# Performance work log

Hardware: AMD Instinct MI355X
Metric: run time of the kernel (lower is better)

Reference implementation:

```python
import jax, jax.numpy as jnp
import numpy as np

BATCH = 64
INPUT_LENGTH = 128
N_TERMINALS = 64
N_NONTERMINALS = 128


def setup_inputs() -> dict:
    key = jax.random.key(0)
    k1, k2, k3 = jax.random.split(key, 3)
    input_tensor = jax.random.uniform(k1, (BATCH, INPUT_LENGTH, N_TERMINALS), dtype=jnp.float32)
    terminal_productions = jax.random.normal(k2, (N_NONTERMINALS, N_TERMINALS), dtype=jnp.float32)
    nonterminal_productions = jax.random.normal(k3, (N_NONTERMINALS, N_NONTERMINALS, N_TERMINALS), dtype=jnp.float32)
    return {
        "input_tensor": input_tensor,
        "terminal_productions": terminal_productions,
        "nonterminal_productions": nonterminal_productions,
    }


def reference(input_tensor, terminal_productions, nonterminal_productions):
    # input_tensor: [B, L, T]
    tp = jax.nn.sigmoid(terminal_productions)            # [N, T]
    ntp = jax.nn.sigmoid(nonterminal_productions)        # [N, N, T]

    # step 0: terminal production choices
    tpc = jnp.einsum('nt,bt->bn', tp, input_tensor[:, 0])  # [B, N]
    out0 = tpc[:, 0]                                        # [B]

    def step(carry, x_i):
        prev_choices, prev_out = carry                     # [B, N], [B]
        # per-batch nonterminal production choice matrix: [B, N, N]
        npc = jnp.clip(jnp.einsum('nmt,bt->bnm', ntp, x_i), 0.0, 1.0)
        cur = jnp.clip(jnp.einsum('bnm,bm->bn', npc, prev_choices), 0.0, 1.0)
        mask = x_i[:, N_TERMINALS - 1]                     # [B]
        out = prev_out * mask + cur[:, 0] * (1.0 - mask)
        return (cur, out), None

    xs = jnp.swapaxes(input_tensor[:, 1:], 0, 1)           # [L-1, B, T]
    (final_choices, final_out), _ = jax.lax.scan(step, (tpc, out0), xs)
    return final_out[:, None]                              # [B, 1]
```

## Files before the change

### kernel.cpp

```cpp
#include <hip/hip_runtime.h>
#include <hip/hip_bf16.h>

typedef unsigned int u32;
typedef unsigned char u8;
typedef _Float16 f16;
typedef f16 f16x2 __attribute__((ext_vector_type(2)));
typedef short s16x8 __attribute__((ext_vector_type(8)));
typedef float f32x4 __attribute__((ext_vector_type(4)));

#define BB 64
#define LL 128
#define TT 64
#define NN 128
#define NM (NN*NN)

__device__ __forceinline__ float sigf(float v) {
    return 1.0f / (1.0f + __expf(-v));
}

__device__ __forceinline__ float clip01(float v) {
    return fminf(fmaxf(v, 0.f), 1.f);
}

__device__ __forceinline__ u32 f2bf(float f) {
    u32 u = __builtin_bit_cast(u32, f);
    return (u + 0x7fffu + ((u >> 16) & 1u)) >> 16;
}

__device__ __forceinline__ float fdot2f(f16x2 wa, f16x2 xa, float ca) {
#if defined(__HIP_DEVICE_COMPILE__) && __has_builtin(__builtin_amdgcn_fdot2)
    return __builtin_amdgcn_fdot2(wa, xa, ca, false);
#else
    return ca + (float)wa[0] * (float)xa[0] + (float)wa[1] * (float)xa[1];
#endif
}

__device__ __forceinline__ u32 ud4(u32 a, u32 b, u32 c) {
#if defined(__HIP_DEVICE_COMPILE__) && __has_builtin(__builtin_amdgcn_udot4)
    return __builtin_amdgcn_udot4(a, b, c, false);
#else
    return c + (a & 255u) * (b & 255u) + ((a >> 8) & 255u) * ((b >> 8) & 255u)
             + ((a >> 16) & 255u) * ((b >> 16) & 255u) + (a >> 24) * (b >> 24);
#endif
}

__global__ __launch_bounds__(256) void pack_w(const float* __restrict__ ntp,
                                              ushort* __restrict__ wpk) {
    const int g = blockIdx.x * 256 + threadIdx.x;
    const int l = g & 63, h = (g >> 6) & 1, i = g >> 7;
    const int row = i * 16 + (l & 15);
    const int t0 = h * 32 + ((l >> 4) << 3);
    const float* src = ntp + row * 64 + t0;
    float4 f0 = *reinterpret_cast<const float4*>(src);
    float4 f1 = *reinterpret_cast<const float4*>(src + 4);
    float v[8] = {f0.x, f0.y, f0.z, f0.w, f1.x, f1.y, f1.z, f1.w};
    u32 o[4];
    #pragma unroll
    for (int q = 0; q < 4; ++q)
        o[q] = f2bf(sigf(v[2 * q])) | (f2bf(sigf(v[2 * q + 1])) << 16);
    uint4 ov; ov.x = o[0]; ov.y = o[1]; ov.z = o[2]; ov.w = o[3];
    *reinterpret_cast<uint4*>(wpk + (size_t)g * 8) = ov;
}

__global__ __launch_bounds__(256) void pack_x(const float* __restrict__ x_all,
                                              ushort* __restrict__ xpk) {
    const int g = blockIdx.x * 256 + threadIdx.x;
    const int l = g & 63, h = (g >> 6) & 1, j = (g >> 7) & 7, b = g >> 10;
    const int s = j * 16 + (l & 15);
    const int t0 = h * 32 + ((l >> 4) << 3);
    const float* src = x_all + ((size_t)b * LL + s) * TT + t0;
    float4 f0 = *reinterpret_cast<const float4*>(src);
    float4 f1 = *reinterpret_cast<const float4*>(src + 4);
    float v[8] = {f0.x, f0.y, f0.z, f0.w, f1.x, f1.y, f1.z, f1.w};
    u32 o[4];
    #pragma unroll
    for (int q = 0; q < 4; ++q)
        o[q] = f2bf(v[2 * q]) | (f2bf(v[2 * q + 1]) << 16);
    uint4 ov; ov.x = o[0]; ov.y = o[1]; ov.z = o[2]; ov.w = o[3];
    *reinterpret_cast<uint4*>(xpk + (size_t)g * 8) = ov;
}

__global__ __launch_bounds__(256) void gemm_mfma(const ushort* __restrict__ wpk,
                                                 const ushort* __restrict__ xpk,
                                                 u8* __restrict__ npc) {
    __shared__ __align__(16) u8 stg[4][16384];
    const int b = blockIdx.x >> 4;
    const int nb = blockIdx.x & 15;
    const int wv = threadIdx.x >> 6, l = threadIdx.x & 63;

    uint4 xf[8][2];
    #pragma unroll
    for (int j = 0; j < 8; ++j)
        #pragma unroll
        for (int h = 0; h < 2; ++h)
            xf[j][h] = *reinterpret_cast<const uint4*>(
                xpk + (size_t)(((b * 8 + j) * 2 + h) * 64 + l) * 8);

    const int c = l & 15, r0 = (l >> 4) * 4;
    u8* stw = stg[wv];
    const int khi  = (nb >> 3) * 8;
    const int nlow = (nb & 7) * 8;

    for (int mg2 = 0; mg2 < 2; ++mg2) {
        const int mg = wv * 2 + mg2;
        #pragma unroll
        for (int n_l = 0; n_l < 8; ++n_l) {
            const int i = (nb * 8 + n_l) * 8 + mg;
            uint4 a0 = *reinterpret_cast<const uint4*>(wpk + (size_t)((i * 2 + 0) * 64 + l) * 8);
            uint4 a1 = *reinterpret_cast<const uint4*>(wpk + (size_t)((i * 2 + 1) * 64 + l) * 8);
            const f32x4 z = {0.f, 0.f, 0.f, 0.f};
            f32x4 acc[8];
            #pragma unroll
            for (int j = 0; j < 8; ++j)
                acc[j] = __builtin_amdgcn_mfma_f32_16x16x32_bf16(
                    __builtin_bit_cast(s16x8, a0), __builtin_bit_cast(s16x8, xf[j][0]), z, 0, 0, 0);
            #pragma unroll
            for (int j = 0; j < 8; ++j)
                acc[j] = __builtin_amdgcn_mfma_f32_16x16x32_bf16(
                    __builtin_bit_cast(s16x8, a1), __builtin_bit_cast(s16x8, xf[j][1]), acc[j], 0, 0, 0);

            const int sk = (((n_l + c) & 7) << 4) + r0;
            #pragma unroll
            for (int j = 0; j < 8; ++j) {
                u32 w = 0;
                #pragma unroll
                for (int r = 0; r < 4; ++r) {
                    float q = clip01(acc[j][r]) * 255.f + 0.5f;
                    w |= ((u32)q) << (8 * r);
                }
                *reinterpret_cast<u32*>(stw + j * 2048 + c * 128 + sk) = w;
            }
        }
        asm volatile("s_waitcnt lgkmcnt(0)" ::: "memory");
        __builtin_amdgcn_sched_barrier(0);

        const int nr = l & 7;
        #pragma unroll
        for (int j = 0; j < 8; ++j) {
            #pragma unroll
            for (int half = 0; half < 2; ++half) {
                const int cc = half * 8 + (l >> 3);
                uint4 v = *reinterpret_cast<const uint4*>(
                    stw + j * 2048 + cc * 128 + (((nr + cc) & 7) << 4));
                *reinterpret_cast<uint4*>(npc + ((size_t)b << 21) + ((size_t)j << 18)
                    + ((size_t)cc << 14) + ((size_t)(mg + khi) << 10)
                    + ((nlow + nr) << 4)) = v;
            }
        }
        asm volatile("s_waitcnt lgkmcnt(0)" ::: "memory");
        __builtin_amdgcn_sched_barrier(0);
    }
}

__global__ __launch_bounds__(256, 1) void recur8(const float* __restrict__ x_all,
                                                 const float* __restrict__ tp,
                                                 const u8* __restrict__ npc,
                                                 float* __restrict__ outp) {
    __shared__ __align__(16) u8 prev_lds[2][NN];
    __shared__ float masks_lds[LL];
    __shared__ float tpc_lds[NN];
    __shared__ float x0_lds[TT];

    const int b = blockIdx.x, tid = threadIdx.x;
    const int n = tid >> 1, h = tid & 1;
    const int koff = (n >> 6) * 8 + h * 4;
    const u8* npcl = npc + ((size_t)b << 21) + (u32)koff * 1024 + (u32)(n & 63) * 16;

    if (tid < 128) masks_lds[tid] = x_all[(size_t)b * 8192 + tid * 64 + 63];
    else if (tid < 192) x0_lds[tid - 128] = x_all[(size_t)b * 8192 + (tid - 128)];
    __syncthreads();

#define LOADSET(R, T) do { \
        int _t = (T) <= 127 ? (T) : 127; \
        const u8* _p = npcl + ((size_t)(_t >> 4) << 18) + ((size_t)(_t & 15) << 14); \
        R[0] = *reinterpret_cast<const uint4*>(_p); \
        R[1] = *reinterpret_cast<const uint4*>(_p + 1024); \
        R[2] = *reinterpret_cast<const uint4*>(_p + 2048); \
        R[3] = *reinterpret_cast<const uint4*>(_p + 3072); \
        asm volatile("" ::: "memory"); \
    } while (0)

    uint4 nA[4], nB[4], nC[4], nD[4];
    LOADSET(nA, 1); LOADSET(nB, 2); LOADSET(nC, 3); LOADSET(nD, 4);

    float out_r = 0.f;
    if (tid < 128) {
        float a = 0.f;
        #pragma unroll
        for (int t4 = 0; t4 < 16; ++t4) {
            float4 xv = *reinterpret_cast<const float4*>(x0_lds + t4 * 4);
            float4 w0 = *reinterpret_cast<const float4*>(tp + tid * 64 + t4 * 4);
            a += sigf(w0.x) * xv.x; a += sigf(w0.y) * xv.y;
            a += sigf(w0.z) * xv.z; a += sigf(w0.w) * xv.w;
        }
        tpc_lds[tid] = a;
        if (tid == 0) out_r = a;
    }
    asm volatile("s_waitcnt lgkmcnt(0)" ::: "memory");
    __builtin_amdgcn_s_barrier();
    __builtin_amdgcn_sched_barrier(0);

    {
        float sf = 0.f;
        #pragma unroll
        for (int j = 0; j < 4; ++j) {
            u32 cw[4] = {nA[j].x, nA[j].y, nA[j].z, nA[j].w};
            #pragma unroll
            for (int w = 0; w < 4; ++w) {
                float4 tv = *reinterpret_cast<const float4*>(
                    tpc_lds + h * 64 + j * 16 + w * 4);
                u32 aw = cw[w];
                sf += (float)(aw & 255u) * tv.x + (float)((aw >> 8) & 255u) * tv.y
                    + (float)((aw >> 16) & 255u) * tv.z + (float)(aw >> 24) * tv.w;
            }
        }
        float tot = sf + __shfl_xor(sf, 1);
        float c0 = clip01(tot * (1.f / 255.f));
        if (h == 0) prev_lds[0][n] = (u8)(c0 * 255.f + 0.5f);
        if (tid == 0) {
            float mk = masks_lds[1];
            out_r = out_r * mk + c0 * (1.f - mk);
        }
        asm volatile("s_waitcnt lgkmcnt(0)" ::: "memory");
        __builtin_amdgcn_s_barrier();
        __builtin_amdgcn_sched_barrier(0);
    }
    LOADSET(nA, 5);

    int p = 0;

#define STEP(R, S) do { \
        uint4 pv[4]; \
        _Pragma("unroll") \
        for (int _q = 0; _q < 4; ++_q) \
            pv[_q] = *reinterpret_cast<const uint4*>(&prev_lds[p][h * 64 + _q * 16]); \
        float mk = masks_lds[(S)]; \
        u32 s0 = 0, s1 = 0; \
        s0 = ud4(R[0].x, pv[0].x, s0); s0 = ud4(R[0].y, pv[0].y, s0); \
        s0 = ud4(R[0].z, pv[0].z, s0); s0 = ud4(R[0].w, pv[0].w, s0); \
        s1 = ud4(R[1].x, pv[1].x, s1); s1 = ud4(R[1].y, pv[1].y, s1); \
        s1 = ud4(R[1].z, pv[1].z, s1); s1 = ud4(R[1].w, pv[1].w, s1); \
        s0 = ud4(R[2].x, pv[2].x, s0); s0 = ud4(R[2].y, pv[2].y, s0); \
        s0 = ud4(R[2].z, pv[2].z, s0); s0 = ud4(R[2].w, pv[2].w, s0); \
        s1 = ud4(R[3].x, pv[3].x, s1); s1 = ud4(R[3].y, pv[3].y, s1); \
        s1 = ud4(R[3].z, pv[3].z, s1); s1 = ud4(R[3].w, pv[3].w, s1); \
        float sf = (float)(s0 + s1); \
        float tot = sf + __shfl_xor(sf, 1); \
        float c0 = fminf(tot * (1.f / 65025.f), 1.f); \
        if (h == 0) prev_lds[p ^ 1][n] = (u8)(c0 * 255.f + 0.5f); \
        if (tid == 0) out_r = out_r * mk + c0 * (1.f - mk); \
        asm volatile("s_waitcnt lgkmcnt(0)" ::: "memory"); \
        __builtin_amdgcn_s_barrier(); \
        __builtin_amdgcn_sched_barrier(0); \
        p ^= 1; \
    } while (0)

    for (int g = 0; g < 31; ++g) {
        const int s = 2 + 4 * g;
        STEP(nB, s);     LOADSET(nB, s + 4);
        STEP(nC, s + 1); LOADSET(nC, s + 5);
        STEP(nD, s + 2); LOADSET(nD, s + 6);
        STEP(nA, s + 3); LOADSET(nA, s + 7);
    }
    STEP(nB, 126);
    STEP(nC, 127);

#undef STEP
#undef LOADSET

    if (tid == 0) outp[b] = out_r;
}

__global__ __launch_bounds__(256) void sig_transpose(const float* __restrict__ ntp,
                                                     u32* __restrict__ out) {
    __shared__ float lds[64 * 65];
    const int nm0 = blockIdx.x * 64;
    const int tid = threadIdx.x;
    #pragma unroll
    for (int it = 0; it < 16; ++it) {
        int idx = it * 256 + tid;
        int r = idx >> 6, c = idx & 63;
        lds[r * 65 + c] = sigf(ntp[(nm0 + r) * 64 + c]);
    }
    __syncthreads();
    #pragma unroll
    for (int it = 0; it < 8; ++it) {
        int o = it * 256 + tid;
        int tpi = o >> 6, r = o & 63;
        f16x2 h;
        h[0] = (f16)lds[r * 65 + 2 * tpi];
        h[1] = (f16)lds[r * 65 + 2 * tpi + 1];
        out[tpi * NM + nm0 + r] = __builtin_bit_cast(u32, h);
    }
}

__global__ __launch_bounds__(1024) void grammar_fused(
    const float* __restrict__ x_all,
    const float* __restrict__ tp,
    const u32*  __restrict__ ntpT2,
    float* __restrict__ outp) {
    __shared__ float x_lds[LL * TT];
    __shared__ float prevbuf[2][NN];
    __shared__ u32 x2_lds[2][32];

    const int b = blockIdx.x;
    const int tid = threadIdx.x;
    const int lane16 = tid & 15;
    const int g = tid >> 4;
    const int mbase = lane16 * 8;

    const float* xb = x_all + b * (LL * TT);
    #pragma unroll
    for (int it = 0; it < 8; ++it) {
        int idx = it * 1024 + tid;
        x_lds[idx] = xb[idx];
    }
    __syncthreads();

    if (tid < NN) {
        float acc = 0.f;
        #pragma unroll 8
        for (int t = 0; t < TT; ++t)
            acc += sigf(tp[tid * TT + t]) * x_lds[t];
        prevbuf[0][tid] = acc;
    }
    __syncthreads();
    float out_r = 0.f;
    if (tid == 0) out_r = prevbuf[0][0];

    int p = 0;
    for (int i0 = 1; i0 < LL; i0 += 2) {
        const int ns = (LL - i0) >= 2 ? 2 : 1;
        if (tid < 64) {
            int s = tid >> 5, tpi = tid & 31;
            f16x2 h;
            if (s < ns) {
                h[0] = (f16)x_lds[(i0 + s) * TT + 2 * tpi];
                h[1] = (f16)x_lds[(i0 + s) * TT + 2 * tpi + 1];
            } else {
                h[0] = (f16)0.f; h[1] = (f16)0.f;
            }
            x2_lds[s][tpi] = __builtin_bit_cast(u32, h);
        }
        __syncthreads();

        float acc[2][2][8];
        #pragma unroll
        for (int k = 0; k < 2; ++k)
            #pragma unroll
            for (int s = 0; s < 2; ++s)
                #pragma unroll
                for (int j = 0; j < 8; ++j) acc[k][s][j] = 0.f;

        #pragma unroll 2
        for (int tpi = 0; tpi < 32; ++tpi) {
            f16x2 xv0 = __builtin_bit_cast(f16x2, x2_lds[0][tpi]);
            f16x2 xv1 = __builtin_bit_cast(f16x2, x2_lds[1][tpi]);
            const u32* base = ntpT2 + tpi * NM + 8 * tid;
            #pragma unroll
            for (int k = 0; k < 2; ++k) {
                uint4 w0 = *reinterpret_cast<const uint4*>(base + 8192 * k);
                uint4 w1 = *reinterpret_cast<const uint4*>(base + 8192 * k + 4);
                u32 wv[8] = {w0.x, w0.y, w0.z, w0.w, w1.x, w1.y, w1.z, w1.w};
                #pragma unroll
                for (int j = 0; j < 8; ++j) {
                    f16x2 w = __builtin_bit_cast(f16x2, wv[j]);
                    acc[k][0][j] = fdot2f(w, xv0, acc[k][0][j]);
                    acc[k][1][j] = fdot2f(w, xv1, acc[k][1][j]);
                }
            }
        }

        for (int s = 0; s < ns; ++s) {
            float4 pv0 = *reinterpret_cast<const float4*>(&prevbuf[p][mbase]);
            float4 pv1 = *reinterpret_cast<const float4*>(&prevbuf[p][mbase + 4]);
            float pvv[8] = {pv0.x, pv0.y, pv0.z, pv0.w, pv1.x, pv1.y, pv1.z, pv1.w};
            #pragma unroll
            for (int k = 0; k < 2; ++k) {
                float part = 0.f;
                #pragma unroll
                for (int j = 0; j < 8; ++j) {
                    float npcv = clip01(acc[k][s][j]);
                    part += npcv * pvv[j];
                }
                part += __shfl_xor(part, 1);
                part += __shfl_xor(part, 2);
                part += __shfl_xor(part, 4);
                part += __shfl_xor(part, 8);
                if (lane16 == 0) {
                    float c = clip01(part);
                    prevbuf[p ^ 1][g + 64 * k] = c;
                    if (tid == 0 && k == 0) {
                        float mask = x_lds[(i0 + s) * TT + 63];
                        out_r = out_r * mask + c * (1.f - mask);
                    }
                }
            }
            p ^= 1;
            __syncthreads();
        }
    }

    if (tid == 0) outp[b] = out_r;
}

extern "C" void kernel_launch(void* const* d_in, const int* in_sizes, int n_in,
                              void* d_out, int out_size, void* d_ws, size_t ws_size,
                              hipStream_t stream) {
    const float* input_tensor = (const float*)d_in[0];
    const float* term_prod    = (const float*)d_in[1];
    const float* nonterm_prod = (const float*)d_in[2];
    float* outp = (float*)d_out;

    const size_t MB = 1024 * 1024;
    const size_t NPC_BYTES = 128 * MB;
    const size_t WPK_BYTES = 2 * MB;
    const size_t XPK_BYTES = 1 * MB;

    if (ws_size >= NPC_BYTES + WPK_BYTES + XPK_BYTES + MB) {
        u8* npcbuf  = (u8*)d_ws;
        ushort* wpk = (ushort*)((char*)d_ws + NPC_BYTES);
        ushort* xpk = (ushort*)((char*)d_ws + NPC_BYTES + WPK_BYTES);
        pack_w<<<512, 256, 0, stream>>>(nonterm_prod, wpk);
        pack_x<<<256, 256, 0, stream>>>(input_tensor, xpk);
        gemm_mfma<<<1024, 256, 0, stream>>>(wpk, xpk, npcbuf);
        recur8<<<BB, 256, 0, stream>>>(input_tensor, term_prod, npcbuf, outp);
    } else {
        u32* ntpT2 = (u32*)d_ws;
        sig_transpose<<<256, 256, 0, stream>>>(nonterm_prod, ntpT2);
        grammar_fused<<<BB, 1024, 0, stream>>>(input_tensor, term_prod, ntpT2, outp);
    }
}
```

Baseline: 81.12 us.

## Quantize npc matrices to 4-bit nibbles and merge pack kernels

Stores the per-step choice matrices as 4-bit values (0..15) instead of 8-bit, halving the 128MB intermediate buffer written by the GEMM and streamed by the recurrence. The recurrence unpacks nibbles with masks/shifts into udot4 against a reordered packed prev vector. It also merges the two packing kernels into one launch. The coarser quantization adds precision error to the recurrent result.

```diff
diff --git a/kernel.cpp b/kernel.cpp
--- a/kernel.cpp
+++ b/kernel.cpp
@@ -44,46 +44,48 @@
 #endif
 }
 
-__global__ __launch_bounds__(256) void pack_w(const float* __restrict__ ntp,
-                                              ushort* __restrict__ wpk) {
-    const int g = blockIdx.x * 256 + threadIdx.x;
-    const int l = g & 63, h = (g >> 6) & 1, i = g >> 7;
-    const int row = i * 16 + (l & 15);
-    const int t0 = h * 32 + ((l >> 4) << 3);
-    const float* src = ntp + row * 64 + t0;
-    float4 f0 = *reinterpret_cast<const float4*>(src);
-    float4 f1 = *reinterpret_cast<const float4*>(src + 4);
-    float v[8] = {f0.x, f0.y, f0.z, f0.w, f1.x, f1.y, f1.z, f1.w};
-    u32 o[4];
-    #pragma unroll
-    for (int q = 0; q < 4; ++q)
-        o[q] = f2bf(sigf(v[2 * q])) | (f2bf(sigf(v[2 * q + 1])) << 16);
-    uint4 ov; ov.x = o[0]; ov.y = o[1]; ov.z = o[2]; ov.w = o[3];
-    *reinterpret_cast<uint4*>(wpk + (size_t)g * 8) = ov;
-}
-
-__global__ __launch_bounds__(256) void pack_x(const float* __restrict__ x_all,
-                                              ushort* __restrict__ xpk) {
-    const int g = blockIdx.x * 256 + threadIdx.x;
-    const int l = g & 63, h = (g >> 6) & 1, j = (g >> 7) & 7, b = g >> 10;
-    const int s = j * 16 + (l & 15);
-    const int t0 = h * 32 + ((l >> 4) << 3);
-    const float* src = x_all + ((size_t)b * LL + s) * TT + t0;
-    float4 f0 = *reinterpret_cast<const float4*>(src);
-    float4 f1 = *reinterpret_cast<const float4*>(src + 4);
-    float v[8] = {f0.x, f0.y, f0.z, f0.w, f1.x, f1.y, f1.z, f1.w};
-    u32 o[4];
-    #pragma unroll
-    for (int q = 0; q < 4; ++q)
-        o[q] = f2bf(v[2 * q]) | (f2bf(v[2 * q + 1]) << 16);
-    uint4 ov; ov.x = o[0]; ov.y = o[1]; ov.z = o[2]; ov.w = o[3];
-    *reinterpret_cast<uint4*>(xpk + (size_t)g * 8) = ov;
+__global__ __launch_bounds__(256) void pack_wx(const float* __restrict__ ntp,
+                                               const float* __restrict__ x_all,
+                                               ushort* __restrict__ wpk,
+                                               ushort* __restrict__ xpk) {
+    const int bid = blockIdx.x;
+    if (bid < 512) {
+        const int g = bid * 256 + threadIdx.x;
+        const int l = g & 63, h = (g >> 6) & 1, i = g >> 7;
+        const int row = i * 16 + (l & 15);
+        const int t0 = h * 32 + ((l >> 4) << 3);
+        const float* src = ntp + row * 64 + t0;
+        float4 f0 = *reinterpret_cast<const float4*>(src);
+        float4 f1 = *reinterpret_cast<const float4*>(src + 4);
+        float v[8] = {f0.x, f0.y, f0.z, f0.w, f1.x, f1.y, f1.z, f1.w};
+        u32 o[4];
+        #pragma unroll
+        for (int q = 0; q < 4; ++q)
+            o[q] = f2bf(sigf(v[2 * q])) | (f2bf(sigf(v[2 * q + 1])) << 16);
+        uint4 ov; ov.x = o[0]; ov.y = o[1]; ov.z = o[2]; ov.w = o[3];
+        *reinterpret_cast<uint4*>(wpk + (size_t)g * 8) = ov;
+    } else {
+        const int g = (bid - 512) * 256 + threadIdx.x;
+        const int l = g & 63, h = (g >> 6) & 1, j = (g >> 7) & 7, b = g >> 10;
+        const int s = j * 16 + (l & 15);
+        const int t0 = h * 32 + ((l >> 4) << 3);
+        const float* src = x_all + ((size_t)b * LL + s) * TT + t0;
+        float4 f0 = *reinterpret_cast<const float4*>(src);
+        float4 f1 = *reinterpret_cast<const float4*>(src + 4);
+        float v[8] = {f0.x, f0.y, f0.z, f0.w, f1.x, f1.y, f1.z, f1.w};
+        u32 o[4];
+        #pragma unroll
+        for (int q = 0; q < 4; ++q)
+            o[q] = f2bf(v[2 * q]) | (f2bf(v[2 * q + 1]) << 16);
+        uint4 ov; ov.x = o[0]; ov.y = o[1]; ov.z = o[2]; ov.w = o[3];
+        *reinterpret_cast<uint4*>(xpk + (size_t)g * 8) = ov;
+    }
 }
 
 __global__ __launch_bounds__(256) void gemm_mfma(const ushort* __restrict__ wpk,
                                                  const ushort* __restrict__ xpk,
                                                  u8* __restrict__ npc) {
-    __shared__ __align__(16) u8 stg[4][16384];
+    __shared__ __align__(16) u8 stg[4][8192];
     const int b = blockIdx.x >> 4;
     const int nb = blockIdx.x & 15;
     const int wv = threadIdx.x >> 6, l = threadIdx.x & 63;
@@ -119,32 +121,32 @@
                 acc[j] = __builtin_amdgcn_mfma_f32_16x16x32_bf16(
                     __builtin_bit_cast(s16x8, a1), __builtin_bit_cast(s16x8, xf[j][1]), acc[j], 0, 0, 0);
 
-            const int sk = (((n_l + c) & 7) << 4) + r0;
+            const int sk8 = ((n_l + c) & 7) << 3;
             #pragma unroll
             for (int j = 0; j < 8; ++j) {
-                u32 w = 0;
-                #pragma unroll
-                for (int r = 0; r < 4; ++r) {
-                    float q = clip01(acc[j][r]) * 255.f + 0.5f;
-                    w |= ((u32)q) << (8 * r);
-                }
-                *reinterpret_cast<u32*>(stw + j * 2048 + c * 128 + sk) = w;
+                u32 q0 = (u32)(clip01(acc[j][0]) * 15.f + 0.5f);
+                u32 q1 = (u32)(clip01(acc[j][1]) * 15.f + 0.5f);
+                u32 q2 = (u32)(clip01(acc[j][2]) * 15.f + 0.5f);
+                u32 q3 = (u32)(clip01(acc[j][3]) * 15.f + 0.5f);
+                u32 hw = (q0 | (q1 << 4)) | ((q2 | (q3 << 4)) << 8);
+                *reinterpret_cast<ushort*>(stw + j * 1024 + c * 64 + sk8 + (r0 >> 1)) = (ushort)hw;
             }
         }
         asm volatile("s_waitcnt lgkmcnt(0)" ::: "memory");
         __builtin_amdgcn_sched_barrier(0);
 
-        const int nr = l & 7;
         #pragma unroll
         for (int j = 0; j < 8; ++j) {
             #pragma unroll
-            for (int half = 0; half < 2; ++half) {
-                const int cc = half * 8 + (l >> 3);
-                uint4 v = *reinterpret_cast<const uint4*>(
-                    stw + j * 2048 + cc * 128 + (((nr + cc) & 7) << 4));
-                *reinterpret_cast<uint4*>(npc + ((size_t)b << 21) + ((size_t)j << 18)
-                    + ((size_t)cc << 14) + ((size_t)(mg + khi) << 10)
-                    + ((nlow + nr) << 4)) = v;
+            for (int r = 0; r < 2; ++r) {
+                const int slot = r * 64 + l;
+                const int cc = slot >> 3;
+                const int nr = slot & 7;
+                uint2 v = *reinterpret_cast<const uint2*>(
+                    stw + j * 1024 + cc * 64 + (((nr + cc) & 7) << 3));
+                *reinterpret_cast<uint2*>(npc + ((size_t)b << 20) + ((size_t)j << 17)
+                    + ((size_t)cc << 13) + ((size_t)(mg + khi) << 9)
+                    + ((nlow + nr) << 3)) = v;
             }
         }
         asm volatile("s_waitcnt lgkmcnt(0)" ::: "memory");
@@ -152,19 +154,19 @@
     }
 }
 
-__global__ __launch_bounds__(256, 1) void recur8(const float* __restrict__ x_all,
+__global__ __launch_bounds__(256, 1) void recur9(const float* __restrict__ x_all,
                                                  const float* __restrict__ tp,
                                                  const u8* __restrict__ npc,
                                                  float* __restrict__ outp) {
-    __shared__ __align__(16) u8 prev_lds[2][NN];
+    __shared__ u32 prev_pk[2][32];
     __shared__ float masks_lds[LL];
     __shared__ float tpc_lds[NN];
     __shared__ float x0_lds[TT];
 
     const int b = blockIdx.x, tid = threadIdx.x;
     const int n = tid >> 1, h = tid & 1;
-    const int koff = (n >> 6) * 8 + h * 4;
-    const u8* npcl = npc + ((size_t)b << 21) + (u32)koff * 1024 + (u32)(n & 63) * 16;
+    const u8* npcl = npc + ((size_t)b << 20)
+                   + ((size_t)((n >> 6) * 8 + h * 4) << 9) + (u32)(n & 63) * 8;
 
     if (tid < 128) masks_lds[tid] = x_all[(size_t)b * 8192 + tid * 64 + 63];
     else if (tid < 192) x0_lds[tid - 128] = x_all[(size_t)b * 8192 + (tid - 128)];
@@ -172,15 +174,15 @@
 
 #define LOADSET(R, T) do { \
         int _t = (T) <= 127 ? (T) : 127; \
-        const u8* _p = npcl + ((size_t)(_t >> 4) << 18) + ((size_t)(_t & 15) << 14); \
-        R[0] = *reinterpret_cast<const uint4*>(_p); \
-        R[1] = *reinterpret_cast<const uint4*>(_p + 1024); \
-        R[2] = *reinterpret_cast<const uint4*>(_p + 2048); \
-        R[3] = *reinterpret_cast<const uint4*>(_p + 3072); \
+        const u8* _p = npcl + ((size_t)(_t >> 4) << 17) + ((size_t)(_t & 15) << 13); \
+        R[0] = *reinterpret_cast<const uint2*>(_p); \
+        R[1] = *reinterpret_cast<const uint2*>(_p + 512); \
+        R[2] = *reinterpret_cast<const uint2*>(_p + 1024); \
+        R[3] = *reinterpret_cast<const uint2*>(_p + 1536); \
         asm volatile("" ::: "memory"); \
     } while (0)
 
-    uint4 nA[4], nB[4], nC[4], nD[4];
+    uint2 nA[4], nB[4], nC[4], nD[4];
     LOADSET(nA, 1); LOADSET(nB, 2); LOADSET(nC, 3); LOADSET(nD, 4);
 
     float out_r = 0.f;
@@ -200,23 +202,31 @@
     __builtin_amdgcn_s_barrier();
     __builtin_amdgcn_sched_barrier(0);
 
+    const int wr_idx  = ((n >> 4) << 1) + ((n >> 3) & 1) + ((n & 1) << 4);
+    const int wr_byte = (n & 7) >> 1;
+
     {
         float sf = 0.f;
         #pragma unroll
-        for (int j = 0; j < 4; ++j) {
-            u32 cw[4] = {nA[j].x, nA[j].y, nA[j].z, nA[j].w};
-            #pragma unroll
-            for (int w = 0; w < 4; ++w) {
-                float4 tv = *reinterpret_cast<const float4*>(
-                    tpc_lds + h * 64 + j * 16 + w * 4);
-                u32 aw = cw[w];
-                sf += (float)(aw & 255u) * tv.x + (float)((aw >> 8) & 255u) * tv.y
-                    + (float)((aw >> 16) & 255u) * tv.z + (float)(aw >> 24) * tv.w;
+        for (int kk = 0; kk < 4; ++kk) {
+            const int base_m = (4 * h + kk) * 16;
+            u32 wlo = nA[kk].x, whi = nA[kk].y;
+            #pragma unroll
+            for (int by = 0; by < 4; ++by) {
+                u32 b0 = (wlo >> (8 * by)) & 0xFFu;
+                sf += (float)(b0 & 15u) * tpc_lds[base_m + 2 * by];
+                sf += (float)(b0 >> 4)  * tpc_lds[base_m + 2 * by + 1];
+                u32 b1 = (whi >> (8 * by)) & 0xFFu;
+                sf += (float)(b1 & 15u) * tpc_lds[base_m + 8 + 2 * by];
+                sf += (float)(b1 >> 4)  * tpc_lds[base_m + 8 + 2 * by + 1];
             }
         }
         float tot = sf + __shfl_xor(sf, 1);
-        float c0 = clip01(tot * (1.f / 255.f));
-        if (h == 0) prev_lds[0][n] = (u8)(c0 * 255.f + 0.5f);
+        float c0 = clip01(tot * (1.f / 15.f));
+        if (h == 0) {
+            u32 q8 = (u32)(c0 * 255.f + 0.5f);
+            ((u8*)&prev_pk[0][wr_idx])[wr_byte] = (u8)q8;
+        }
         if (tid == 0) {
             float mk = masks_lds[1];
             out_r = out_r * mk + c0 * (1.f - mk);
@@ -230,24 +240,29 @@
     int p = 0;
 
 #define STEP(R, S) do { \
-        uint4 pv[4]; \
+        uint4 pe0 = *reinterpret_cast<const uint4*>(&prev_pk[p][8 * h]); \
+        uint4 pe1 = *reinterpret_cast<const uint4*>(&prev_pk[p][8 * h + 4]); \
+        uint4 po0 = *reinterpret_cast<const uint4*>(&prev_pk[p][16 + 8 * h]); \
+        uint4 po1 = *reinterpret_cast<const uint4*>(&prev_pk[p][16 + 8 * h + 4]); \
+        u32 PE[8] = {pe0.x, pe0.y, pe0.z, pe0.w, pe1.x, pe1.y, pe1.z, pe1.w}; \
+        u32 PO[8] = {po0.x, po0.y, po0.z, po0.w, po1.x, po1.y, po1.z, po1.w}; \
+        float mk = masks_lds[(S)]; \
+        u32 ae = 0, ao = 0; \
         _Pragma("unroll") \
-        for (int _q = 0; _q < 4; ++_q) \
-            pv[_q] = *reinterpret_cast<const uint4*>(&prev_lds[p][h * 64 + _q * 16]); \
-        float mk = masks_lds[(S)]; \
-        u32 s0 = 0, s1 = 0; \
-        s0 = ud4(R[0].x, pv[0].x, s0); s0 = ud4(R[0].y, pv[0].y, s0); \
-        s0 = ud4(R[0].z, pv[0].z, s0); s0 = ud4(R[0].w, pv[0].w, s0); \
-        s1 = ud4(R[1].x, pv[1].x, s1); s1 = ud4(R[1].y, pv[1].y, s1); \
-        s1 = ud4(R[1].z, pv[1].z, s1); s1 = ud4(R[1].w, pv[1].w, s1); \
-        s0 = ud4(R[2].x, pv[2].x, s0); s0 = ud4(R[2].y, pv[2].y, s0); \
-        s0 = ud4(R[2].z, pv[2].z, s0); s0 = ud4(R[2].w, pv[2].w, s0); \
-        s1 = ud4(R[3].x, pv[3].x, s1); s1 = ud4(R[3].y, pv[3].y, s1); \
-        s1 = ud4(R[3].z, pv[3].z, s1); s1 = ud4(R[3].w, pv[3].w, s1); \
-        float sf = (float)(s0 + s1); \
+        for (int _kk = 0; _kk < 4; ++_kk) { \
+            u32 _w0 = R[_kk].x, _w1 = R[_kk].y; \
+            ae = ud4(_w0 & 0x0F0F0F0Fu, PE[2 * _kk], ae); \
+            ao = ud4((_w0 >> 4) & 0x0F0F0F0Fu, PO[2 * _kk], ao); \
+            ae = ud4(_w1 & 0x0F0F0F0Fu, PE[2 * _kk + 1], ae); \
+            ao = ud4((_w1 >> 4) & 0x0F0F0F0Fu, PO[2 * _kk + 1], ao); \
+        } \
+        float sf = (float)(ae + ao); \
         float tot = sf + __shfl_xor(sf, 1); \
-        float c0 = fminf(tot * (1.f / 65025.f), 1.f); \
-        if (h == 0) prev_lds[p ^ 1][n] = (u8)(c0 * 255.f + 0.5f); \
+        float c0 = fminf(tot * (1.f / 3825.f), 1.f); \
+        if (h == 0) { \
+            u32 q8 = (u32)(c0 * 255.f + 0.5f); \
+            ((u8*)&prev_pk[p ^ 1][wr_idx])[wr_byte] = (u8)q8; \
+        } \
         if (tid == 0) out_r = out_r * mk + c0 * (1.f - mk); \
         asm volatile("s_waitcnt lgkmcnt(0)" ::: "memory"); \
         __builtin_amdgcn_s_barrier(); \
@@ -413,7 +428,7 @@
     float* outp = (float*)d_out;
 
     const size_t MB = 1024 * 1024;
-    const size_t NPC_BYTES = 128 * MB;
+    const size_t NPC_BYTES = 64 * MB;
     const size_t WPK_BYTES = 2 * MB;
     const size_t XPK_BYTES = 1 * MB;
 
@@ -421,10 +436,9 @@
         u8* npcbuf  = (u8*)d_ws;
         ushort* wpk = (ushort*)((char*)d_ws + NPC_BYTES);
         ushort* xpk = (ushort*)((char*)d_ws + NPC_BYTES + WPK_BYTES);
-        pack_w<<<512, 256, 0, stream>>>(nonterm_prod, wpk);
-        pack_x<<<256, 256, 0, stream>>>(input_tensor, xpk);
+        pack_wx<<<768, 256, 0, stream>>>(nonterm_prod, input_tensor, wpk, xpk);
         gemm_mfma<<<1024, 256, 0, stream>>>(wpk, xpk, npcbuf);
-        recur8<<<BB, 256, 0, stream>>>(input_tensor, term_prod, npcbuf, outp);
+        recur9<<<BB, 256, 0, stream>>>(input_tensor, term_prod, npcbuf, outp);
     } else {
         u32* ntpT2 = (u32*)d_ws;
         sig_transpose<<<256, 256, 0, stream>>>(nonterm_prod, ntpT2);
```

Measured after the change: 77.77 us, median of 2. 1.04x faster.
